# Kernel tuning notes

Hardware: AMD Instinct MI355X
Metric: run time of the kernel (lower is better)

Reference implementation:

```python
import jax, jax.numpy as jnp
import numpy as np

N = 50000
IN_F = 256
HID = 32
HEADS = 4
NEG_SLOPE = 0.2


def _gat_layer(x, edge_index, W, a_src, a_dst, bias):
    # x: [N, Fin]; W: [Fin, H*C]; a_src/a_dst: [H, C]; bias: [H*C]
    n = x.shape[0]
    H, C = a_src.shape
    h = (x @ W).reshape(n, H, C)                     # [N, H, C]
    alpha_src = jnp.einsum('nhc,hc->nh', h, a_src)   # [N, H]
    alpha_dst = jnp.einsum('nhc,hc->nh', h, a_dst)   # [N, H]
    src, dst = edge_index[0], edge_index[1]
    logits = alpha_src[src] + alpha_dst[dst]         # [E, H]
    logits = jax.nn.leaky_relu(logits, negative_slope=NEG_SLOPE)
    # segment softmax over edges grouped by destination node
    seg_max = jax.ops.segment_max(logits, dst, num_segments=n)
    seg_max = jnp.where(jnp.isfinite(seg_max), seg_max, 0.0)
    e = jnp.exp(logits - seg_max[dst])               # [E, H]
    denom = jax.ops.segment_sum(e, dst, num_segments=n)  # [N, H]
    attn = e / (denom[dst] + 1e-16)                  # [E, H]
    msg = h[src] * attn[:, :, None]                  # [E, H, C]
    out = jax.ops.segment_sum(msg, dst, num_segments=n)  # [N, H, C]
    return out.reshape(n, H * C) + bias


def _add_self_loops(edge_index, n):
    # PyG GATConv default add_self_loops=True
    loops = jnp.arange(n, dtype=edge_index.dtype)
    return jnp.concatenate([edge_index, jnp.stack([loops, loops])], axis=1)


def setup_inputs() -> dict:
    key = jax.random.key(0)
    ks = jax.random.split(key, 10)
    x = jax.random.normal(ks[0], (N, IN_F), dtype=jnp.float32)
    edge_index = jax.random.randint(ks[1], (2, 800000), 0, N, dtype=jnp.int64)
    d1 = HEADS * HID
    s1 = 1.0 / np.sqrt(IN_F)
    W1 = jax.random.normal(ks[2], (IN_F, d1), dtype=jnp.float32) * s1
    a_src1 = jax.random.normal(ks[3], (HEADS, HID), dtype=jnp.float32) * 0.1
    a_dst1 = jax.random.normal(ks[4], (HEADS, HID), dtype=jnp.float32) * 0.1
    b1 = jnp.zeros((d1,), dtype=jnp.float32)
    s2 = 1.0 / np.sqrt(d1)
    W2 = jax.random.normal(ks[5], (d1, d1), dtype=jnp.float32) * s2
    a_src2 = jax.random.normal(ks[6], (HEADS, HID), dtype=jnp.float32) * 0.1
    a_dst2 = jax.random.normal(ks[7], (HEADS, HID), dtype=jnp.float32) * 0.1
    b2 = jnp.zeros((d1,), dtype=jnp.float32)
    return {"x": x, "edge_index": edge_index, "W1": W1, "a_src1": a_src1,
            "a_dst1": a_dst1, "b1": b1, "W2": W2, "a_src2": a_src2,
            "a_dst2": a_dst2, "b2": b2}


def reference(x, edge_index, W1, a_src1, a_dst1, b1, W2, a_src2, a_dst2, b2):
    # Inference mode: dropout layers are identity.
    ei = _add_self_loops(edge_index, x.shape[0])
    h = _gat_layer(x, ei, W1, a_src1, a_dst1, b1)
    h = jax.nn.elu(h)
    h = _gat_layer(h, ei, W2, a_src2, a_dst2, b2)
    return h
```

## Files before the change

kernel.cpp:

```cpp
#include <hip/hip_runtime.h>
#include <hip/hip_fp16.h>
#include <math.h>

#define HEADS 4
#define HID 32
#define D1 128
#define IN_FEAT 256
#define NEG_SLOPE 0.2f
#define CAP 64
#define AGG_NODES 8
#define EPT 8

#define WTS_STRIDE_H 72
#define HTS_STRIDE_H 136
#define SMEM_BYTES (128 * 272)

typedef _Float16 half8 __attribute__((ext_vector_type(8)));
typedef float f32x4 __attribute__((ext_vector_type(4)));
typedef long long ll2 __attribute__((ext_vector_type(2)));

static inline int ceil_div(int a, int b) { return (a + b - 1) / b; }

static __device__ inline float2 unpack_h2(unsigned int v) {
    __half2 h = __builtin_bit_cast(__half2, v);
    return __half22float2(h);
}

static __device__ inline void fma_mix_lo(float& a, unsigned int h2, float w) {
    asm("v_fma_mix_f32 %0, %1, %2, %0 op_sel:[0,0,0] op_sel_hi:[1,0,0]"
        : "+v"(a) : "v"(h2), "v"(w));
}
static __device__ inline void fma_mix_hi(float& a, unsigned int h2, float w) {
    asm("v_fma_mix_f32 %0, %1, %2, %0 op_sel:[1,0,0] op_sel_hi:[1,0,0]"
        : "+v"(a) : "v"(h2), "v"(w));
}

__global__ void init_prep(const unsigned int* __restrict__ raw, int* __restrict__ flag,
                          const float* __restrict__ W1, _Float16* __restrict__ WT1,
                          const float* __restrict__ W2, _Float16* __restrict__ WT2,
                          int* __restrict__ cnt, int N) {
    int i = blockIdx.x * blockDim.x + threadIdx.x;
    if (i < N) cnt[i] = 0;
    if (i < IN_FEAT * D1) {
        int k = i >> 7, n = i & 127;
        WT1[(size_t)n * IN_FEAT + k] = (_Float16)W1[i];
    }
    if (i < D1 * D1) {
        int k = i >> 7, n = i & 127;
        WT2[(size_t)n * D1 + k] = (_Float16)W2[i];
    }
    if (blockIdx.x == 0 && threadIdx.x < 64) {
        unsigned int hi = raw[2 * threadIdx.x + 1];
        unsigned long long b = __ballot(hi != 0u);
        if (threadIdx.x == 0) *flag = (b == 0ULL) ? 1 : 0;
    }
}

__device__ void scatter_body(int sbid, const void* __restrict__ raw,
                             const int* __restrict__ flag,
                             int* __restrict__ cnt,
                             unsigned short* __restrict__ slots,
                             int E, int N, int Sg) {
    const int grp  = sbid & 7;
    const int rank = sbid >> 3;
    const int nrank = (Sg - grp + 7) >> 3;
    const int range = (N + 7) >> 3;
    const int lo = grp * range;
    const int hi = min(lo + range, N);
    const bool wide = (*flag != 0);
    const int NC = (E + 2047) >> 11;

    for (int c = rank; c < NC; c += nrank) {
        const int e0 = (c << 11) + (int)threadIdx.x * EPT;
        int s[EPT], d[EPT];
        bool val[EPT];
        if (e0 + EPT <= E) {
            if (wide) {
                const ll2* ps = (const ll2*)((const long long*)raw + e0);
                const ll2* pd = (const ll2*)((const long long*)raw + E + e0);
#pragma unroll
                for (int i = 0; i < EPT / 2; ++i) {
                    ll2 a = ps[i], b = pd[i];
                    s[2 * i] = (int)a[0]; s[2 * i + 1] = (int)a[1];
                    d[2 * i] = (int)b[0]; d[2 * i + 1] = (int)b[1];
                }
            } else {
                const int4* ps = (const int4*)((const int*)raw + e0);
                const int4* pd = (const int4*)((const int*)raw + E + e0);
#pragma unroll
                for (int i = 0; i < EPT / 4; ++i) {
                    int4 a = ps[i], b = pd[i];
                    s[4 * i] = a.x; s[4 * i + 1] = a.y; s[4 * i + 2] = a.z; s[4 * i + 3] = a.w;
                    d[4 * i] = b.x; d[4 * i + 1] = b.y; d[4 * i + 2] = b.z; d[4 * i + 3] = b.w;
                }
            }
#pragma unroll
            for (int i = 0; i < EPT; ++i) val[i] = true;
        } else {
#pragma unroll
            for (int i = 0; i < EPT; ++i) {
                int e = e0 + i;
                val[i] = (e < E);
                if (val[i]) {
                    if (wide) { s[i] = (int)((const long long*)raw)[e]; d[i] = (int)((const long long*)raw)[E + e]; }
                    else      { s[i] = ((const int*)raw)[e];            d[i] = ((const int*)raw)[E + e]; }
                } else { s[i] = 0; d[i] = -1; }
            }
        }
#pragma unroll
        for (int i = 0; i < EPT; ++i) {
            if (val[i] && d[i] >= lo && d[i] < hi) {
                int pos = atomicAdd(&cnt[d[i]], 1);
                if (pos < CAP) slots[(size_t)d[i] * CAP + pos] = (unsigned short)s[i];
            }
        }
    }
}

template <int AF16>
__device__ void gemm_body(char* smem, int bid, const void* __restrict__ Ain,
                          const _Float16* __restrict__ WT,
                          _Float16* __restrict__ Hout,
                          const float* __restrict__ a_src,
                          const float* __restrict__ a_dst,
                          float* __restrict__ asrc_out,
                          float* __restrict__ adst_out,
                          int M, int K) {
    const int tid = threadIdx.x;
    const int wave = tid >> 6, lane = tid & 63;
    const int quad = lane >> 4, l16 = lane & 15;
    const int row0 = bid * 128;
    const int m0 = min(row0 + wave * 32 + l16, M - 1);
    const int m1 = min(row0 + wave * 32 + 16 + l16, M - 1);
    const float*    Af = (const float*)Ain;
    const _Float16* Ah = (const _Float16*)Ain;
    const uint4* WTg = (const uint4*)WT;
    const int K8 = K >> 3;

    f32x4 acc[2][8];
#pragma unroll
    for (int r = 0; r < 2; ++r)
#pragma unroll
        for (int c = 0; c < 8; ++c) acc[r][c] = (f32x4){0.f, 0.f, 0.f, 0.f};

    for (int kb = 0; kb < K; kb += 64) {
        __syncthreads();
#pragma unroll
        for (int i = 0; i < 4; ++i) {
            int c = tid + i * 256;
            int n = c >> 3, j = c & 7;
            uint4 v = WTg[(size_t)n * K8 + (kb >> 3) + j];
            *(uint4*)(smem + n * 144 + j * 16) = v;
        }
        __syncthreads();
#pragma unroll
        for (int kc = 0; kc < 2; ++kc) {
            int k0 = kb + kc * 32 + quad * 8;
            half8 a0f, a1f;
            if (AF16) {
                a0f = *(const half8*)(Ah + (size_t)m0 * K + k0);
                a1f = *(const half8*)(Ah + (size_t)m1 * K + k0);
            } else {
                float4 x0 = *(const float4*)(Af + (size_t)m0 * K + k0);
                float4 x1 = *(const float4*)(Af + (size_t)m0 * K + k0 + 4);
                float4 y0 = *(const float4*)(Af + (size_t)m1 * K + k0);
                float4 y1 = *(const float4*)(Af + (size_t)m1 * K + k0 + 4);
                a0f[0] = (_Float16)x0.x; a0f[1] = (_Float16)x0.y;
                a0f[2] = (_Float16)x0.z; a0f[3] = (_Float16)x0.w;
                a0f[4] = (_Float16)x1.x; a0f[5] = (_Float16)x1.y;
                a0f[6] = (_Float16)x1.z; a0f[7] = (_Float16)x1.w;
                a1f[0] = (_Float16)y0.x; a1f[1] = (_Float16)y0.y;
                a1f[2] = (_Float16)y0.z; a1f[3] = (_Float16)y0.w;
                a1f[4] = (_Float16)y1.x; a1f[5] = (_Float16)y1.y;
                a1f[6] = (_Float16)y1.z; a1f[7] = (_Float16)y1.w;
            }
#pragma unroll
            for (int c = 0; c < 8; ++c) {
                half8 bf = *(const half8*)(smem + (c * 16 + l16) * 144 + kc * 64 + quad * 16);
                acc[0][c] = __builtin_amdgcn_mfma_f32_16x16x32_f16(a0f, bf, acc[0][c], 0, 0, 0);
                acc[1][c] = __builtin_amdgcn_mfma_f32_16x16x32_f16(a1f, bf, acc[1][c], 0, 0, 0);
            }
        }
    }

    __syncthreads();
    _Float16* hts = (_Float16*)smem;
#pragma unroll
    for (int r = 0; r < 2; ++r)
#pragma unroll
        for (int c = 0; c < 8; ++c)
#pragma unroll
            for (int g = 0; g < 4; ++g) {
                int row = wave * 32 + r * 16 + quad * 4 + g;
                hts[row * HTS_STRIDE_H + c * 16 + l16] = (_Float16)acc[r][c][g];
            }
    __syncthreads();

    const int r = tid >> 1;
    const int part = tid & 1;
    const int grow = row0 + r;
    const uint4* hrow = (const uint4*)(smem + r * 272 + part * 128);
    if (grow < M) {
        uint4* dv = (uint4*)(Hout + (size_t)grow * 128 + part * 64);
#pragma unroll
        for (int i = 0; i < 8; ++i) dv[i] = hrow[i];
    }
#pragma unroll
    for (int t = 0; t < 2; ++t) {
        int hh = part * 2 + t;
        const uint4* hv = (const uint4*)(smem + r * 272 + hh * 64);
        const float4* as4 = (const float4*)(a_src + hh * HID);
        const float4* ad4 = (const float4*)(a_dst + hh * HID);
        float ps = 0.f, pd = 0.f;
#pragma unroll
        for (int b = 0; b < 4; ++b) {
            uint4 u = hv[b];
            float2 f0 = unpack_h2(u.x), f1 = unpack_h2(u.y);
            float2 f2 = unpack_h2(u.z), f3 = unpack_h2(u.w);
            float4 s0 = as4[b * 2], s1 = as4[b * 2 + 1];
            float4 d0 = ad4[b * 2], d1 = ad4[b * 2 + 1];
            ps += f0.x * s0.x + f0.y * s0.y + f1.x * s0.z + f1.y * s0.w
                + f2.x * s1.x + f2.y * s1.y + f3.x * s1.z + f3.y * s1.w;
            pd += f0.x * d0.x + f0.y * d0.y + f1.x * d0.z + f1.y * d0.w
                + f2.x * d1.x + f2.y * d1.y + f3.x * d1.z + f3.y * d1.w;
        }
        if (grow < M) {
            asrc_out[grow * 4 + hh] = ps;
            adst_out[grow * 4 + hh] = pd;
        }
    }
}

template <int AF16>
__global__ __launch_bounds__(256) void gemm128(const void* __restrict__ Ain,
                                               const _Float16* __restrict__ WT,
                                               _Float16* __restrict__ Hout,
                                               const float* __restrict__ a_src,
                                               const float* __restrict__ a_dst,
                                               float* __restrict__ asrc_out,
                                               float* __restrict__ adst_out,
                                               int M, int K) {
    __shared__ __align__(16) char smem[SMEM_BYTES];
    gemm_body<AF16>(smem, blockIdx.x, Ain, WT, Hout, a_src, a_dst,
                    asrc_out, adst_out, M, K);
}

template <int AF16>
__global__ __launch_bounds__(256) void gemm128_scatter(const void* __restrict__ Ain,
                                                       const _Float16* __restrict__ WT,
                                                       _Float16* __restrict__ Hout,
                                                       const float* __restrict__ a_src,
                                                       const float* __restrict__ a_dst,
                                                       float* __restrict__ asrc_out,
                                                       float* __restrict__ adst_out,
                                                       int M, int K,
                                                       const void* __restrict__ raw,
                                                       const int* __restrict__ flag,
                                                       int* __restrict__ cnt,
                                                       unsigned short* __restrict__ slots,
                                                       int E, int Sg) {
    __shared__ __align__(16) char smem[SMEM_BYTES];
    if ((int)blockIdx.x < Sg) {
        scatter_body(blockIdx.x, raw, flag, cnt, slots, E, M, Sg);
        return;
    }
    gemm_body<AF16>(smem, blockIdx.x - Sg, Ain, WT, Hout, a_src, a_dst,
                    asrc_out, adst_out, M, K);
}

__global__ __launch_bounds__(256) void aggregate(const _Float16* __restrict__ hb,
                                                 const int* __restrict__ cnt,
                                                 const unsigned short* __restrict__ slots,
                                                 const float* __restrict__ asrc,
                                                 const float* __restrict__ adst,
                                                 const float* __restrict__ bias,
                                                 float* __restrict__ out32,
                                                 _Float16* __restrict__ out16,
                                                 int N, int apply_elu) {
    const int w = threadIdx.x >> 6;
    const int lane = threadIdx.x & 63;
    const int half = lane >> 5;
    const int hl = lane & 31;
    const int idx = w * 2 + half;
    const int node = blockIdx.x * AGG_NODES + idx;
    const bool live = (node < N);

    __shared__ float wsh[AGG_NODES][CAP][4];
    __shared__ int ssh[AGG_NODES][CAP];

    int cntE = 0, count = 1;
    if (live) {
        cntE = min(cnt[node], CAP - 1);
        count = cntE + 1;
    }
    const unsigned short* nslots = slots + (size_t)node * CAP;

    float4 ad4 = live ? *(const float4*)&adst[node * 4] : make_float4(0.f, 0.f, 0.f, 0.f);

    const bool v0 = live && (hl < count);
    const bool v1 = live && (hl + 32 < count);
    float lv0[4] = {-1e30f, -1e30f, -1e30f, -1e30f};
    float lv1[4] = {-1e30f, -1e30f, -1e30f, -1e30f};
    if (v0) {
        int src = (hl < cntE) ? (int)nslots[hl] : node;
        ssh[idx][hl] = src << 8;
        float4 as4 = *(const float4*)&asrc[src * 4];
        float t0 = as4.x + ad4.x, t1 = as4.y + ad4.y;
        float t2 = as4.z + ad4.z, t3 = as4.w + ad4.w;
        lv0[0] = t0 > 0.f ? t0 : NEG_SLOPE * t0;
        lv0[1] = t1 > 0.f ? t1 : NEG_SLOPE * t1;
        lv0[2] = t2 > 0.f ? t2 : NEG_SLOPE * t2;
        lv0[3] = t3 > 0.f ? t3 : NEG_SLOPE * t3;
    }
    if (v1) {
        int j = hl + 32;
        int src = (j < cntE) ? (int)nslots[j] : node;
        ssh[idx][j] = src << 8;
        float4 as4 = *(const float4*)&asrc[src * 4];
        float t0 = as4.x + ad4.x, t1 = as4.y + ad4.y;
        float t2 = as4.z + ad4.z, t3 = as4.w + ad4.w;
        lv1[0] = t0 > 0.f ? t0 : NEG_SLOPE * t0;
        lv1[1] = t1 > 0.f ? t1 : NEG_SLOPE * t1;
        lv1[2] = t2 > 0.f ? t2 : NEG_SLOPE * t2;
        lv1[3] = t3 > 0.f ? t3 : NEG_SLOPE * t3;
    }

    float m[4];
#pragma unroll
    for (int h = 0; h < 4; ++h) m[h] = fmaxf(lv0[h], lv1[h]);
#pragma unroll
    for (int off = 16; off >= 1; off >>= 1)
#pragma unroll
        for (int h = 0; h < 4; ++h)
            m[h] = fmaxf(m[h], __shfl_xor(m[h], off, 64));

    float e0[4], e1[4], sum[4];
#pragma unroll
    for (int h = 0; h < 4; ++h) {
        e0[h] = v0 ? __expf(lv0[h] - m[h]) : 0.f;
        e1[h] = v1 ? __expf(lv1[h] - m[h]) : 0.f;
        sum[h] = e0[h] + e1[h];
    }
#pragma unroll
    for (int off = 16; off >= 1; off >>= 1)
#pragma unroll
        for (int h = 0; h < 4; ++h)
            sum[h] += __shfl_xor(sum[h], off, 64);

    if (v0) {
        float4 w4;
        w4.x = e0[0] / (sum[0] + 1e-16f);
        w4.y = e0[1] / (sum[1] + 1e-16f);
        w4.z = e0[2] / (sum[2] + 1e-16f);
        w4.w = e0[3] / (sum[3] + 1e-16f);
        *(float4*)&wsh[idx][hl][0] = w4;
    }
    if (v1) {
        float4 w4;
        w4.x = e1[0] / (sum[0] + 1e-16f);
        w4.y = e1[1] / (sum[1] + 1e-16f);
        w4.z = e1[2] / (sum[2] + 1e-16f);
        w4.w = e1[3] / (sum[3] + 1e-16f);
        *(float4*)&wsh[idx][hl + 32][0] = w4;
    }
    __syncthreads();

    const int q = hl >> 4;
    const int sub = hl & 15;
    const int hh = sub >> 2;
    const char* hbase = (const char*)hb;
    const int sub16 = sub * 16;

    float acc[8];
#pragma unroll
    for (int i = 0; i < 8; ++i) acc[i] = 0.f;

#define ROW_FMA(u, wt)                                   \
    do {                                                 \
        fma_mix_lo(acc[0], (u).x, (wt));                 \
        fma_mix_hi(acc[1], (u).x, (wt));                 \
        fma_mix_lo(acc[2], (u).y, (wt));                 \
        fma_mix_hi(acc[3], (u).y, (wt));                 \
        fma_mix_lo(acc[4], (u).z, (wt));                 \
        fma_mix_hi(acc[5], (u).z, (wt));                 \
        fma_mix_lo(acc[6], (u).w, (wt));                 \
        fma_mix_hi(acc[7], (u).w, (wt));                 \
    } while (0)

    if (live) {
        int j = q;
        if (j + 2 < count) {
            int o0 = ssh[idx][j], o1 = ssh[idx][j + 2];
            float w0 = wsh[idx][j][hh], w1 = wsh[idx][j + 2][hh];
            uint4 u0 = *(const uint4*)(hbase + (unsigned)(o0 + sub16));
            uint4 u1 = *(const uint4*)(hbase + (unsigned)(o1 + sub16));
            for (j += 4; j + 2 < count; j += 4) {
                int t0 = ssh[idx][j], t1 = ssh[idx][j + 2];
                float x0 = wsh[idx][j][hh], x1 = wsh[idx][j + 2][hh];
                uint4 n0 = *(const uint4*)(hbase + (unsigned)(t0 + sub16));
                uint4 n1 = *(const uint4*)(hbase + (unsigned)(t1 + sub16));
                ROW_FMA(u0, w0);
                ROW_FMA(u1, w1);
                u0 = n0; u1 = n1; w0 = x0; w1 = x1;
            }
            ROW_FMA(u0, w0);
            ROW_FMA(u1, w1);
        }
        if (j < count) {
            int o0 = ssh[idx][j];
            float w0 = wsh[idx][j][hh];
            uint4 u0 = *(const uint4*)(hbase + (unsigned)(o0 + sub16));
            ROW_FMA(u0, w0);
        }
    }
#undef ROW_FMA

#pragma unroll
    for (int i = 0; i < 8; ++i) acc[i] += __shfl_xor(acc[i], 16, 64);

    if (live && q == 0) {
        int ch8 = sub * 8;
        float o[8];
#pragma unroll
        for (int i = 0; i < 8; ++i) o[i] = acc[i] + bias[ch8 + i];
        if (apply_elu) {
#pragma unroll
            for (int i = 0; i < 8; ++i) o[i] = o[i] > 0.f ? o[i] : __expf(o[i]) - 1.f;
        }
        if (out16) {
            __align__(16) _Float16 t[8];
#pragma unroll
            for (int i = 0; i < 8; ++i) t[i] = (_Float16)o[i];
            *(uint4*)&out16[(size_t)node * D1 + ch8] = *(const uint4*)t;
        } else {
            *(float4*)&out32[(size_t)node * D1 + ch8]     = make_float4(o[0], o[1], o[2], o[3]);
            *(float4*)&out32[(size_t)node * D1 + ch8 + 4] = make_float4(o[4], o[5], o[6], o[7]);
        }
    }
}

extern "C" void kernel_launch(void* const* d_in, const int* in_sizes, int n_in,
                              void* d_out, int out_size, void* d_ws, size_t ws_size,
                              hipStream_t stream) {
    const float* x      = (const float*)d_in[0];
    const void*  e_raw  = d_in[1];
    const float* W1     = (const float*)d_in[2];
    const float* a_src1 = (const float*)d_in[3];
    const float* a_dst1 = (const float*)d_in[4];
    const float* b1     = (const float*)d_in[5];
    const float* W2     = (const float*)d_in[6];
    const float* a_src2 = (const float*)d_in[7];
    const float* a_dst2 = (const float*)d_in[8];
    const float* b2     = (const float*)d_in[9];

    const int N  = in_sizes[0] / IN_FEAT;
    const int E  = in_sizes[1] / 2;
    float* out = (float*)d_out;

    char* ws = (char*)d_ws;
    size_t woff = 0;
    auto walloc = [&](size_t bytes) -> char* {
        char* p = ws + woff;
        woff = (woff + bytes + 255) & ~(size_t)255;
        return p;
    };
    int*   flag  = (int*)walloc(4);
    int*   cnt   = (int*)walloc((size_t)N * 4);
    unsigned short* slots = (unsigned short*)walloc((size_t)N * CAP * 2);
    float* asrc  = (float*)walloc((size_t)N * HEADS * 4);
    float* adst  = (float*)walloc((size_t)N * HEADS * 4);
    _Float16* hb  = (_Float16*)walloc((size_t)N * D1 * 2);
    _Float16* o16 = (_Float16*)walloc((size_t)N * D1 * 2);
    _Float16* WT1 = (_Float16*)walloc((size_t)IN_FEAT * D1 * 2);
    _Float16* WT2 = (_Float16*)walloc((size_t)D1 * D1 * 2);

    const int Gg = ceil_div(N, 128);
    const int Sg = ceil_div(E, 256 * EPT);
    const int Ga = ceil_div(N, AGG_NODES);
    const int initN = (N > IN_FEAT * D1) ? N : IN_FEAT * D1;

    init_prep<<<ceil_div(initN, 256), 256, 0, stream>>>(
        (const unsigned int*)e_raw, flag, W1, WT1, W2, WT2, cnt, N);
    gemm128_scatter<0><<<Sg + Gg, 256, 0, stream>>>(
        x, WT1, hb, a_src1, a_dst1, asrc, adst, N, IN_FEAT,
        e_raw, flag, cnt, slots, E, Sg);
    aggregate<<<Ga, 256, 0, stream>>>(hb, cnt, slots, asrc, adst, b1, nullptr, o16, N, 1);
    gemm128<1><<<Gg, 256, 0, stream>>>(o16, WT2, hb, a_src2, a_dst2, asrc, adst, N, D1);
    aggregate<<<Ga, 256, 0, stream>>>(hb, cnt, slots, asrc, adst, b2, out, nullptr, N, 0);
}
```

Baseline: 253.1 us.

## Restructure edge scatter into per-block multi-pass ranges and deepen aggregate gather unroll

The scatter phase no longer assigns each block a destination-node group with a strided loop over edge chunks. Each block now loads one chunk of edges once and makes 8 passes over destination ranges, with a block barrier between passes, so atomics stay localized without rereading the edge list. The aggregate inner loop now keeps four row loads in flight instead of two, with a predicated tail, to raise memory-level parallelism. Risks: the scatter grid size Sg must now cover all edges (one 2048-edge chunk per block), which the host must guarantee, and the deeper unroll raises register pressure.

```diff
diff --git a/kernel.cpp b/kernel.cpp
--- a/kernel.cpp
+++ b/kernel.cpp
@@ -9,6 +9,7 @@
 #define NEG_SLOPE 0.2f
 #define CAP 64
 #define AGG_NODES 8
+#define NPASS 8
 #define EPT 8
 
 #define WTS_STRIDE_H 72
@@ -60,53 +61,49 @@
                              const int* __restrict__ flag,
                              int* __restrict__ cnt,
                              unsigned short* __restrict__ slots,
-                             int E, int N, int Sg) {
-    const int grp  = sbid & 7;
-    const int rank = sbid >> 3;
-    const int nrank = (Sg - grp + 7) >> 3;
-    const int range = (N + 7) >> 3;
-    const int lo = grp * range;
-    const int hi = min(lo + range, N);
+                             int E, int N) {
+    const int e0 = (sbid * 256 + (int)threadIdx.x) * EPT;
     const bool wide = (*flag != 0);
-    const int NC = (E + 2047) >> 11;
-
-    for (int c = rank; c < NC; c += nrank) {
-        const int e0 = (c << 11) + (int)threadIdx.x * EPT;
-        int s[EPT], d[EPT];
-        bool val[EPT];
-        if (e0 + EPT <= E) {
-            if (wide) {
-                const ll2* ps = (const ll2*)((const long long*)raw + e0);
-                const ll2* pd = (const ll2*)((const long long*)raw + E + e0);
-#pragma unroll
-                for (int i = 0; i < EPT / 2; ++i) {
-                    ll2 a = ps[i], b = pd[i];
-                    s[2 * i] = (int)a[0]; s[2 * i + 1] = (int)a[1];
-                    d[2 * i] = (int)b[0]; d[2 * i + 1] = (int)b[1];
-                }
-            } else {
-                const int4* ps = (const int4*)((const int*)raw + e0);
-                const int4* pd = (const int4*)((const int*)raw + E + e0);
-#pragma unroll
-                for (int i = 0; i < EPT / 4; ++i) {
-                    int4 a = ps[i], b = pd[i];
-                    s[4 * i] = a.x; s[4 * i + 1] = a.y; s[4 * i + 2] = a.z; s[4 * i + 3] = a.w;
-                    d[4 * i] = b.x; d[4 * i + 1] = b.y; d[4 * i + 2] = b.z; d[4 * i + 3] = b.w;
-                }
-            }
-#pragma unroll
-            for (int i = 0; i < EPT; ++i) val[i] = true;
+    int s[EPT], d[EPT];
+    bool val[EPT];
+    if (e0 + EPT <= E) {
+        if (wide) {
+            const ll2* ps = (const ll2*)((const long long*)raw + e0);
+            const ll2* pd = (const ll2*)((const long long*)raw + E + e0);
+#pragma unroll
+            for (int i = 0; i < EPT / 2; ++i) {
+                ll2 a = ps[i], b = pd[i];
+                s[2 * i] = (int)a[0]; s[2 * i + 1] = (int)a[1];
+                d[2 * i] = (int)b[0]; d[2 * i + 1] = (int)b[1];
+            }
         } else {
-#pragma unroll
-            for (int i = 0; i < EPT; ++i) {
-                int e = e0 + i;
-                val[i] = (e < E);
-                if (val[i]) {
-                    if (wide) { s[i] = (int)((const long long*)raw)[e]; d[i] = (int)((const long long*)raw)[E + e]; }
-                    else      { s[i] = ((const int*)raw)[e];            d[i] = ((const int*)raw)[E + e]; }
-                } else { s[i] = 0; d[i] = -1; }
-            }
-        }
+            const int4* ps = (const int4*)((const int*)raw + e0);
+            const int4* pd = (const int4*)((const int*)raw + E + e0);
+#pragma unroll
+            for (int i = 0; i < EPT / 4; ++i) {
+                int4 a = ps[i], b = pd[i];
+                s[4 * i] = a.x; s[4 * i + 1] = a.y; s[4 * i + 2] = a.z; s[4 * i + 3] = a.w;
+                d[4 * i] = b.x; d[4 * i + 1] = b.y; d[4 * i + 2] = b.z; d[4 * i + 3] = b.w;
+            }
+        }
+#pragma unroll
+        for (int i = 0; i < EPT; ++i) val[i] = true;
+    } else {
+#pragma unroll
+        for (int i = 0; i < EPT; ++i) {
+            int e = e0 + i;
+            val[i] = (e < E);
+            if (val[i]) {
+                if (wide) { s[i] = (int)((const long long*)raw)[e]; d[i] = (int)((const long long*)raw)[E + e]; }
+                else      { s[i] = ((const int*)raw)[e];            d[i] = ((const int*)raw)[E + e]; }
+            } else { s[i] = 0; d[i] = -1; }
+        }
+    }
+
+    const int range = (N + NPASS - 1) / NPASS;
+    int lo = 0;
+    for (int p = 0; p < NPASS; ++p, lo += range) {
+        const int hi = lo + range;
 #pragma unroll
         for (int i = 0; i < EPT; ++i) {
             if (val[i] && d[i] >= lo && d[i] < hi) {
@@ -114,6 +111,7 @@
                 if (pos < CAP) slots[(size_t)d[i] * CAP + pos] = (unsigned short)s[i];
             }
         }
+        __syncthreads();
     }
 }
 
@@ -261,7 +259,7 @@
                                                        int E, int Sg) {
     __shared__ __align__(16) char smem[SMEM_BYTES];
     if ((int)blockIdx.x < Sg) {
-        scatter_body(blockIdx.x, raw, flag, cnt, slots, E, M, Sg);
+        scatter_body(blockIdx.x, raw, flag, cnt, slots, E, M);
         return;
     }
     gemm_body<AF16>(smem, blockIdx.x - Sg, Ain, WT, Hout, a_src, a_dst,
@@ -375,6 +373,7 @@
 #pragma unroll
     for (int i = 0; i < 8; ++i) acc[i] = 0.f;
 
+#define LDROW(off) (*(const uint4*)(hbase + (unsigned)((off) + sub16)))
 #define ROW_FMA(u, wt)                                   \
     do {                                                 \
         fma_mix_lo(acc[0], (u).x, (wt));                 \
@@ -389,31 +388,44 @@
 
     if (live) {
         int j = q;
-        if (j + 2 < count) {
-            int o0 = ssh[idx][j], o1 = ssh[idx][j + 2];
+        if (j + 6 < count) {
+            int o0 = ssh[idx][j], o1 = ssh[idx][j + 2], o2 = ssh[idx][j + 4], o3 = ssh[idx][j + 6];
             float w0 = wsh[idx][j][hh], w1 = wsh[idx][j + 2][hh];
-            uint4 u0 = *(const uint4*)(hbase + (unsigned)(o0 + sub16));
-            uint4 u1 = *(const uint4*)(hbase + (unsigned)(o1 + sub16));
-            for (j += 4; j + 2 < count; j += 4) {
-                int t0 = ssh[idx][j], t1 = ssh[idx][j + 2];
+            float w2 = wsh[idx][j + 4][hh], w3 = wsh[idx][j + 6][hh];
+            uint4 u0 = LDROW(o0), u1 = LDROW(o1), u2 = LDROW(o2), u3 = LDROW(o3);
+            for (j += 8; j + 6 < count; j += 8) {
+                int p0 = ssh[idx][j], p1 = ssh[idx][j + 2], p2 = ssh[idx][j + 4], p3 = ssh[idx][j + 6];
                 float x0 = wsh[idx][j][hh], x1 = wsh[idx][j + 2][hh];
-                uint4 n0 = *(const uint4*)(hbase + (unsigned)(t0 + sub16));
-                uint4 n1 = *(const uint4*)(hbase + (unsigned)(t1 + sub16));
-                ROW_FMA(u0, w0);
-                ROW_FMA(u1, w1);
-                u0 = n0; u1 = n1; w0 = x0; w1 = x1;
-            }
-            ROW_FMA(u0, w0);
-            ROW_FMA(u1, w1);
-        }
-        if (j < count) {
-            int o0 = ssh[idx][j];
-            float w0 = wsh[idx][j][hh];
-            uint4 u0 = *(const uint4*)(hbase + (unsigned)(o0 + sub16));
-            ROW_FMA(u0, w0);
+                float x2 = wsh[idx][j + 4][hh], x3 = wsh[idx][j + 6][hh];
+                uint4 n0 = LDROW(p0), n1 = LDROW(p1), n2 = LDROW(p2), n3 = LDROW(p3);
+                ROW_FMA(u0, w0); ROW_FMA(u1, w1); ROW_FMA(u2, w2); ROW_FMA(u3, w3);
+                u0 = n0; u1 = n1; u2 = n2; u3 = n3;
+                w0 = x0; w1 = x1; w2 = x2; w3 = x3;
+            }
+            const bool b0 = j < count, b1 = j + 2 < count, b2 = j + 4 < count;
+            uint4 t0 = {0, 0, 0, 0}, t1 = {0, 0, 0, 0}, t2 = {0, 0, 0, 0};
+            float y0 = 0.f, y1 = 0.f, y2 = 0.f;
+            if (b0) { t0 = LDROW(ssh[idx][j]);     y0 = wsh[idx][j][hh]; }
+            if (b1) { t1 = LDROW(ssh[idx][j + 2]); y1 = wsh[idx][j + 2][hh]; }
+            if (b2) { t2 = LDROW(ssh[idx][j + 4]); y2 = wsh[idx][j + 4][hh]; }
+            ROW_FMA(u0, w0); ROW_FMA(u1, w1); ROW_FMA(u2, w2); ROW_FMA(u3, w3);
+            if (b0) ROW_FMA(t0, y0);
+            if (b1) ROW_FMA(t1, y1);
+            if (b2) ROW_FMA(t2, y2);
+        } else {
+            const bool b0 = j < count, b1 = j + 2 < count, b2 = j + 4 < count;
+            uint4 t0 = {0, 0, 0, 0}, t1 = {0, 0, 0, 0}, t2 = {0, 0, 0, 0};
+            float y0 = 0.f, y1 = 0.f, y2 = 0.f;
+            if (b0) { t0 = LDROW(ssh[idx][j]);     y0 = wsh[idx][j][hh]; }
+            if (b1) { t1 = LDROW(ssh[idx][j + 2]); y1 = wsh[idx][j + 2][hh]; }
+            if (b2) { t2 = LDROW(ssh[idx][j + 4]); y2 = wsh[idx][j + 4][hh]; }
+            if (b0) ROW_FMA(t0, y0);
+            if (b1) ROW_FMA(t1, y1);
+            if (b2) ROW_FMA(t2, y2);
         }
     }
 #undef ROW_FMA
+#undef LDROW
 
 #pragma unroll
     for (int i = 0; i < 8; ++i) acc[i] += __shfl_xor(acc[i], 16, 64);
```

New measurement: 244.1 us, median of 2. 3.5% less time.
